# Kernel tuning notes

Hardware: AMD Instinct MI355X
Metric: run time of the kernel (lower is better)

The kernel has to match this reference:

```python
import jax, jax.numpy as jnp
import numpy as np

NUM_NODES = 100000
NUM_EDGES = 1600000
NUM_GRAPHS = 64
D_IN = 128
HID = 256
N_ATTR = 8
D_OUT = 1


def setup_inputs() -> dict:
    key = jax.random.key(0)
    ks = jax.random.split(key, 16)
    x = jax.random.normal(ks[0], (NUM_NODES, D_IN), dtype=jnp.float32)
    edge_index = jax.random.randint(ks[1], (2, NUM_EDGES), 0, NUM_NODES, dtype=jnp.int64)
    batch = jnp.sort(jax.random.randint(ks[2], (NUM_NODES,), 0, NUM_GRAPHS, dtype=jnp.int64))
    graph_attr = jax.random.normal(ks[3], (NUM_GRAPHS, N_ATTR), dtype=jnp.float32)
    def lin(k, fi, fo):
        s = 1.0 / np.sqrt(fi)
        return jax.random.uniform(k, (fi, fo), jnp.float32, -s, s)
    # SAGEConv: lin_l (applied to aggregated neighbors, has bias) + lin_r (root, no bias)
    W1l = lin(ks[4], D_IN, HID); b1 = jnp.zeros((HID,), jnp.float32)
    W1r = lin(ks[5], D_IN, HID)
    W2l = lin(ks[6], HID, HID); b2 = jnp.zeros((HID,), jnp.float32)
    W2r = lin(ks[7], HID, HID)
    Wf1 = lin(ks[8], HID + N_ATTR, HID); bf1 = jnp.zeros((HID,), jnp.float32)
    Wf2 = lin(ks[9], HID, D_OUT); bf2 = jnp.zeros((D_OUT,), jnp.float32)
    return {"x": x, "edge_index": edge_index, "batch": batch, "graph_attr": graph_attr,
            "W1l": W1l, "b1": b1, "W1r": W1r, "W2l": W2l, "b2": b2, "W2r": W2r,
            "Wf1": Wf1, "bf1": bf1, "Wf2": Wf2, "bf2": bf2}


def _mean_agg(h, src, dst, num_segments):
    # gather source features, scatter-mean into destination nodes
    s = jax.ops.segment_sum(h[src], dst, num_segments=num_segments)
    cnt = jax.ops.segment_sum(jnp.ones((src.shape[0], 1), h.dtype), dst, num_segments=num_segments)
    return s / jnp.maximum(cnt, 1.0)


def _sage(h, src, dst, Wl, b, Wr):
    agg = _mean_agg(h, src, dst, h.shape[0])
    return agg @ Wl + b + h @ Wr


def reference(x, edge_index, batch, graph_attr, W1l, b1, W1r, W2l, b2, W2r, Wf1, bf1, Wf2, bf2):
    src, dst = edge_index[0], edge_index[1]
    h = jax.nn.relu(_sage(x, src, dst, W1l, b1, W1r))
    h = _sage(h, src, dst, W2l, b2, W2r)
    # global mean pool over graphs
    gsum = jax.ops.segment_sum(h, batch, num_segments=NUM_GRAPHS)
    gcnt = jax.ops.segment_sum(jnp.ones((h.shape[0], 1), h.dtype), batch, num_segments=NUM_GRAPHS)
    g = gsum / jnp.maximum(gcnt, 1.0)
    g = jnp.concatenate([g, graph_attr.reshape(-1, N_ATTR)], axis=1)
    g = jax.nn.relu(g @ Wf1 + bf1)
    return g @ Wf2 + bf2
```

## Files before the change

### kernel.cpp

```cpp
#include <hip/hip_runtime.h>
#include <stdint.h>

#define NN 100000
#define NE 1600000
#define NG 64
#define DIN 128
#define HID 256
#define NATTR 8
#define NBK 391
#define CAP 6144
#define PCH 4096
#define BWW 25000
#define CB 12756
#define AEL 2048

typedef unsigned short u16;
typedef __attribute__((ext_vector_type(8))) short s16x8;
typedef __attribute__((ext_vector_type(4))) float f32x4;
typedef __attribute__((ext_vector_type(2))) float f32x2;
typedef __attribute__((ext_vector_type(4))) unsigned u32x4;

__device__ __forceinline__ int imaxi(int a, int b) { return a > b ? a : b; }
__device__ __forceinline__ u16 f2bf(float f) {
    unsigned u = __float_as_uint(f);
    return (u16)((u + 0x7fffu + ((u >> 16) & 1u)) >> 16);
}
__device__ __forceinline__ void gload16(const void* g, void* l) {
    __builtin_amdgcn_global_load_lds((const __attribute__((address_space(1))) void*)g,
                                     (__attribute__((address_space(3))) void*)l, 16, 0, 0);
}


__global__ void k_prep(const float4* __restrict__ x4, ushort4* __restrict__ xb4,
                       const float* __restrict__ W1l, const float* __restrict__ W1r,
                       u16* __restrict__ W1lt, u16* __restrict__ W1rt,
                       float4* __restrict__ P84, const int* __restrict__ batch,
                       int* __restrict__ goff, int* __restrict__ gcnt,
                       int* __restrict__ cursor) {
    int b = blockIdx.x, t = threadIdx.x;
    if (b < CB) {
        int i = b * 256 + t;
        const int NX4 = NN * DIN / 4;
        if (i < NX4) {
            float4 v = x4[i];
            ushort4 o;
            o.x = f2bf(v.x); o.y = f2bf(v.y); o.z = f2bf(v.z); o.w = f2bf(v.w);
            xb4[i] = o;
        } else {
            int j = i - NX4;
            if (j < 32768) {
                int n = j >> 7, k = j & 127;
                W1lt[j] = f2bf(W1l[k * HID + n]);
            } else if (j < 65536) {
                int jj = j - 32768;
                int n = jj >> 7, k = jj & 127;
                W1rt[jj] = f2bf(W1r[k * HID + n]);
            }
        }
    } else if (b < CB + 256) {
        int i = (b - CB) * 256 + t;
        P84[i] = make_float4(0.f, 0.f, 0.f, 0.f);
    } else {
        for (int i = t; i < NBK; i += 256) cursor[i] = 0;
        int g = t;
        if (g <= NG) {
            int lo = 0, hi = NN;
            while (lo < hi) {
                int mid = (lo + hi) >> 1;
                if (batch[mid] < g) lo = mid + 1; else hi = mid;
            }
            goff[g] = lo;
        }
        __syncthreads();
        if (g < NG) gcnt[g] = goff[g + 1] - goff[g];
    }
}


__global__ __launch_bounds__(256) void k_part(const int* __restrict__ ei,
                                              int* __restrict__ cursor,
                                              unsigned* __restrict__ pairs) {
    __shared__ unsigned spk[PCH];
    __shared__ unsigned short sbk[PCH];
    __shared__ int hist[NBK], gb[NBK];
    __shared__ int sc[512];
    int t = threadIdx.x;
    int c0 = blockIdx.x * PCH;
    int n = NE - c0; if (n > PCH) n = PCH;
    for (int i = t; i < NBK; i += 256) hist[i] = 0;
    __syncthreads();
    unsigned mypk[16]; unsigned short mybk[16]; int myoff[16];
#pragma unroll
    for (int j = 0; j < 16; j++) {
        int i = t + j * 256;
        myoff[j] = -1;
        if (i < n) {
            int e = c0 + i;
            unsigned d = (unsigned)__builtin_nontemporal_load(&ei[NE + e]);
            unsigned s = (unsigned)__builtin_nontemporal_load(&ei[e]);
            unsigned bk = d >> 8;
            mypk[j] = ((d & 255u) << 24) | s;
            mybk[j] = (unsigned short)bk;
            myoff[j] = atomicAdd(&hist[bk], 1);
        }
    }
    __syncthreads();
    sc[t] = (t < NBK) ? hist[t] : 0;
    sc[t + 256] = (t + 256 < NBK) ? hist[t + 256] : 0;
    __syncthreads();
    for (int off = 1; off < 512; off <<= 1) {
        int v0 = (t >= off) ? sc[t - off] : 0;
        int v1 = (t + 256 >= off) ? sc[t + 256 - off] : 0;
        __syncthreads();
        sc[t] += v0; sc[t + 256] += v1;
        __syncthreads();
    }
    if (t < NBK && hist[t] > 0) gb[t] = atomicAdd(&cursor[t], hist[t]);
    if (t + 256 < NBK && hist[t + 256] > 0)
        gb[t + 256] = atomicAdd(&cursor[t + 256], hist[t + 256]);
    __syncthreads();
#pragma unroll
    for (int j = 0; j < 16; j++) {
        if (myoff[j] >= 0) {
            int bk = mybk[j];
            int pos = sc[bk] - hist[bk] + myoff[j];
            spk[pos] = mypk[j];
            sbk[pos] = (unsigned short)bk;
        }
    }
    __syncthreads();
    for (int i = t; i < n; i += 256) {
        int bk = sbk[i];
        int local = gb[bk] + (i - (sc[bk] - hist[bk]));
        pairs[(size_t)bk * CAP + local] = spk[i];
    }
}


__global__ __launch_bounds__(256) void k_csr(const unsigned* __restrict__ pairs,
                                             const int* __restrict__ cursor,
                                             int* __restrict__ rowptr,
                                             unsigned* __restrict__ col) {
    __shared__ unsigned colL[CAP];
    __shared__ int csc[512];
    __shared__ int cnt[256], cur[256], sc[256];
    int b = blockIdx.x, t = threadIdx.x;
    csc[t] = (t < NBK) ? cursor[t] : 0;
    csc[t + 256] = (t + 256 < NBK) ? cursor[t + 256] : 0;
    __syncthreads();
    for (int off = 1; off < 512; off <<= 1) {
        int v0 = (t >= off) ? csc[t - off] : 0;
        int v1 = (t + 256 >= off) ? csc[t + 256 - off] : 0;
        __syncthreads();
        csc[t] += v0; csc[t + 256] += v1;
        __syncthreads();
    }
    int obase = (b == 0) ? 0 : csc[b - 1];
    int ecnt = cursor[b];
    const unsigned* pp = pairs + (size_t)b * CAP;
    cnt[t] = 0;
    __syncthreads();
    for (int i = t; i < ecnt; i += 256)
        atomicAdd(&cnt[pp[i] >> 24], 1);
    __syncthreads();
    sc[t] = cnt[t];
    __syncthreads();
    for (int off = 1; off < 256; off <<= 1) {
        int v = (t >= off) ? sc[t - off] : 0;
        __syncthreads();
        sc[t] += v;
        __syncthreads();
    }
    int lr = sc[t] - cnt[t];
    cur[t] = lr;
    int node = (b << 8) + t;
    if (node < NN) rowptr[node] = obase + lr;
    if (b == NBK - 1 && t == 0) rowptr[NN] = obase + ecnt;
    __syncthreads();
    for (int i = t; i < ecnt; i += 256) {
        unsigned p = pp[i];
        int dl = p >> 24;
        int pos = atomicAdd(&cur[dl], 1);
        int dd = cnt[dl]; if (dd > 32767) dd = 32767;
        colL[pos] = ((unsigned)dd << 17) | (p & 0xFFFFFFu);
    }
    __syncthreads();
    for (int i = t; i < ecnt; i += 256)
        col[obase + i] = colL[i];
}


__global__ __launch_bounds__(256) void k_agg(const uint4* __restrict__ xb4,
                                             uint4* __restrict__ agg4,
                                             const int* __restrict__ rowptr,
                                             const unsigned* __restrict__ col) {
    __shared__ unsigned scol[AEL];
    int t = threadIdx.x;
    int base = blockIdx.x * 4;
    int node = base + (t >> 6);
    int lane = t & 63;
    int qtr = lane >> 4, li = lane & 15;
    int s = rowptr[node], e = rowptr[node + 1];
    int bs = rowptr[base], be = rowptr[base + 4];
    int bn = be - bs;
    bool inl = bn <= AEL;
    if (inl)
        for (int j = t; j < bn; j += 256) scol[j] = col[bs + j];
    __syncthreads();

    f32x2 b01 = {0.f, 0.f}, b23 = {0.f, 0.f}, b45 = {0.f, 0.f}, b67 = {0.f, 0.f};

#define ACC8(V) do { \
        f32x2 p; \
        p[0] = __uint_as_float((V).x << 16); p[1] = __uint_as_float((V).x & 0xffff0000u); b01 += p; \
        p[0] = __uint_as_float((V).y << 16); p[1] = __uint_as_float((V).y & 0xffff0000u); b23 += p; \
        p[0] = __uint_as_float((V).z << 16); p[1] = __uint_as_float((V).z & 0xffff0000u); b45 += p; \
        p[0] = __uint_as_float((V).w << 16); p[1] = __uint_as_float((V).w & 0xffff0000u); b67 += p; \
    } while (0)

#define CL(X) scol[(X) - bs]
#define CG(X) col[X]
#define AGG_BODY(CIDX) do { \
        for (; i + 16 <= e; i += 16) { \
            unsigned c0 = (CIDX(i + qtr)) & 0x1FFFFu; \
            unsigned c1 = (CIDX(i + 4 + qtr)) & 0x1FFFFu; \
            unsigned c2 = (CIDX(i + 8 + qtr)) & 0x1FFFFu; \
            unsigned c3 = (CIDX(i + 12 + qtr)) & 0x1FFFFu; \
            uint4 w0 = xb4[(size_t)c0 * 16 + li]; \
            uint4 w1 = xb4[(size_t)c1 * 16 + li]; \
            uint4 w2 = xb4[(size_t)c2 * 16 + li]; \
            uint4 w3 = xb4[(size_t)c3 * 16 + li]; \
            ACC8(w0); ACC8(w1); ACC8(w2); ACC8(w3); \
        } \
        if (i + 8 <= e) { \
            unsigned c0 = (CIDX(i + qtr)) & 0x1FFFFu; \
            unsigned c1 = (CIDX(i + 4 + qtr)) & 0x1FFFFu; \
            uint4 w0 = xb4[(size_t)c0 * 16 + li]; \
            uint4 w1 = xb4[(size_t)c1 * 16 + li]; \
            ACC8(w0); ACC8(w1); \
            i += 8; \
        } \
        if (i + 4 <= e) { \
            unsigned c = (CIDX(i + qtr)) & 0x1FFFFu; \
            uint4 wv = xb4[(size_t)c * 16 + li]; \
            ACC8(wv); \
            i += 4; \
        } \
        if (i + qtr < e) { \
            unsigned c = (CIDX(i + qtr)) & 0x1FFFFu; \
            uint4 wv = xb4[(size_t)c * 16 + li]; \
            ACC8(wv); \
        } \
    } while (0)

    int i = s;
    if (inl) { AGG_BODY(CL); } else { AGG_BODY(CG); }
#undef AGG_BODY
#undef CL
#undef CG
#undef ACC8

    float a0 = b01[0], a1 = b01[1], a2 = b23[0], a3 = b23[1];
    float a4 = b45[0], a5 = b45[1], a6 = b67[0], a7 = b67[1];
    a0 += __shfl_xor(a0, 16); a1 += __shfl_xor(a1, 16);
    a2 += __shfl_xor(a2, 16); a3 += __shfl_xor(a3, 16);
    a4 += __shfl_xor(a4, 16); a5 += __shfl_xor(a5, 16);
    a6 += __shfl_xor(a6, 16); a7 += __shfl_xor(a7, 16);
    a0 += __shfl_xor(a0, 32); a1 += __shfl_xor(a1, 32);
    a2 += __shfl_xor(a2, 32); a3 += __shfl_xor(a3, 32);
    a4 += __shfl_xor(a4, 32); a5 += __shfl_xor(a5, 32);
    a6 += __shfl_xor(a6, 32); a7 += __shfl_xor(a7, 32);
    if (qtr == 0) {
        float inv = 1.f / (float)imaxi(e - s, 1);
        u32x4 ov;
        ov[0] = (((unsigned)f2bf(a1 * inv)) << 16) | (unsigned)f2bf(a0 * inv);
        ov[1] = (((unsigned)f2bf(a3 * inv)) << 16) | (unsigned)f2bf(a2 * inv);
        ov[2] = (((unsigned)f2bf(a5 * inv)) << 16) | (unsigned)f2bf(a4 * inv);
        ov[3] = (((unsigned)f2bf(a7 * inv)) << 16) | (unsigned)f2bf(a6 * inv);
        __builtin_nontemporal_store(ov, (u32x4*)&agg4[(size_t)node * 16 + li]);
    }
}


__global__ __launch_bounds__(512) void k_gemm1(
    const u16* __restrict__ agg1, const u16* __restrict__ xb,
    const u16* __restrict__ W1lt, const u16* __restrict__ W1rt,
    const float* __restrict__ b1, u16* __restrict__ h1t) {
    __shared__ u16 As[128][32];
    __shared__ u16 Bs[256][32];
    int t = threadIdx.x;
    int m0 = blockIdx.x * 128;
    int wave = t >> 6, lane = t & 63;
    int wm = wave & 1, wn = wave >> 1;
    int lm = lane & 15, quad = lane >> 4;
    int ar = t >> 2, aq = t & 3;
    f32x4 acc[4][4] = {};
    const u16* Ap = agg1;
    const u16* Bp = W1lt;
#pragma unroll
    for (int ph = 0; ph < 2; ph++) {
        for (int k0 = 0; k0 < DIN; k0 += 32) {
            gload16(Ap + (size_t)(m0 + ar) * DIN + k0 + aq * 8, &As[wave * 16][0]);
#pragma unroll
            for (int i = 0; i < 2; i++) {
                int r = (t + i * 512) >> 2;
                gload16(Bp + (size_t)r * DIN + k0 + aq * 8, &Bs[wave * 16 + i * 128][0]);
            }
            __syncthreads();
            s16x8 af[4], bfr[4];
#pragma unroll
            for (int i = 0; i < 4; i++) {
                af[i]  = *(const s16x8*)&As[wm * 64 + i * 16 + lm][quad * 8];
                bfr[i] = *(const s16x8*)&Bs[wn * 64 + i * 16 + lm][quad * 8];
            }
#pragma unroll
            for (int mi = 0; mi < 4; mi++)
#pragma unroll
                for (int ni = 0; ni < 4; ni++)
                    acc[mi][ni] = __builtin_amdgcn_mfma_f32_16x16x32_bf16(
                        af[mi], bfr[ni], acc[mi][ni], 0, 0, 0);
            __syncthreads();
        }
        Ap = xb; Bp = W1rt;
    }
#pragma unroll
    for (int ni = 0; ni < 4; ni++) {
        int colf = wn * 64 + ni * 16 + lm;
        float bias = b1[colf];
#pragma unroll
        for (int mi = 0; mi < 4; mi++) {
            int row = m0 + wm * 64 + mi * 16 + quad * 4;
            if (row < NN) {
                ushort4 o;
                o.x = f2bf(fmaxf(acc[mi][ni][0] + bias, 0.f));
                o.y = f2bf(fmaxf(acc[mi][ni][1] + bias, 0.f));
                o.z = f2bf(fmaxf(acc[mi][ni][2] + bias, 0.f));
                o.w = f2bf(fmaxf(acc[mi][ni][3] + bias, 0.f));
                *(ushort4*)(h1t + (size_t)colf * NN + row) = o;
            }
        }
    }
}


__global__ __launch_bounds__(256) void k_bw(
    const int* __restrict__ rowptr, const unsigned* __restrict__ col,
    const int* __restrict__ goff, u16* __restrict__ Wbt) {
    int b = blockIdx.x, t = threadIdx.x;
    if (b < 256) {
        __shared__ float bins[BWW];
        int g = b >> 2, w = b & 3;
        int lo = w * BWW;
        for (int i = t; i < BWW; i += 256) bins[i] = 0.f;
        __syncthreads();
        int ebeg = rowptr[goff[g]], eend = rowptr[goff[g + 1]];
        for (int i = ebeg + t; i < eend; i += 256) {
            unsigned c = col[i];
            unsigned sl = (c & 0x1FFFFu) - lo;
            if (sl < (unsigned)BWW) atomicAdd(&bins[sl], 1.0f / (float)(c >> 17));
        }
        __syncthreads();
        u16* out = Wbt + (size_t)g * NN + lo;
        for (int k = t; k < BWW / 4; k += 256) {
            ushort4 o;
            o.x = f2bf(bins[4 * k + 0]); o.y = f2bf(bins[4 * k + 1]);
            o.z = f2bf(bins[4 * k + 2]); o.w = f2bf(bins[4 * k + 3]);
            *(ushort4*)(out + 4 * k) = o;
        }
    } else {
        int g = b - 256;
        int a = goff[g], bnd = goff[g + 1];
        u16* out = Wbt + (size_t)(NG + g) * NN;
        for (int k = t; k < NN / 4; k += 256) {
            int c0 = 4 * k;
            ushort4 o;
            o.x = (c0 + 0 >= a && c0 + 0 < bnd) ? 0x3F80 : 0;
            o.y = (c0 + 1 >= a && c0 + 1 < bnd) ? 0x3F80 : 0;
            o.z = (c0 + 2 >= a && c0 + 2 < bnd) ? 0x3F80 : 0;
            o.w = (c0 + 3 >= a && c0 + 3 < bnd) ? 0x3F80 : 0;
            *(ushort4*)(out + c0) = o;
        }
    }
}


#define KCHUNK 512

__global__ __launch_bounds__(512) void k_poolg(
    const u16* __restrict__ Wbt, const u16* __restrict__ h1t, float* __restrict__ P8) {
    __shared__ u16 As[128][32];
    __shared__ u16 Bs[256][32];
    int t = threadIdx.x;
    int kbase = blockIdx.x * KCHUNK;
    int krem = NN - kbase;
    int ksteps = (krem < KCHUNK ? krem : KCHUNK) >> 5;
    int wave = t >> 6, lane = t & 63;
    int wm = wave & 1, wn = wave >> 1;
    int lm = lane & 15, quad = lane >> 4;
    int ar = t >> 2, aq = t & 3;
    float* P = P8 + (size_t)(blockIdx.x & 7) * 128 * HID;
    f32x4 acc[4][4] = {};
    for (int ks = 0; ks < ksteps; ks++) {
        int k0 = kbase + ks * 32;
        gload16(Wbt + (size_t)ar * NN + k0 + aq * 8, &As[wave * 16][0]);
#pragma unroll
        for (int i = 0; i < 2; i++) {
            int r = (t + i * 512) >> 2;
            gload16(h1t + (size_t)r * NN + k0 + aq * 8, &Bs[wave * 16 + i * 128][0]);
        }
        __syncthreads();
        s16x8 af[4], bfr[4];
#pragma unroll
        for (int i = 0; i < 4; i++) {
            af[i]  = *(const s16x8*)&As[wm * 64 + i * 16 + lm][quad * 8];
            bfr[i] = *(const s16x8*)&Bs[wn * 64 + i * 16 + lm][quad * 8];
        }
#pragma unroll
        for (int mi = 0; mi < 4; mi++)
#pragma unroll
            for (int ni = 0; ni < 4; ni++)
                acc[mi][ni] = __builtin_amdgcn_mfma_f32_16x16x32_bf16(
                    af[mi], bfr[ni], acc[mi][ni], 0, 0, 0);
        __syncthreads();
    }
#pragma unroll
    for (int mi = 0; mi < 4; mi++)
#pragma unroll
        for (int ni = 0; ni < 4; ni++) {
            int gcol = wm * 64 + mi * 16 + quad * 4;
            int feat = wn * 64 + ni * 16 + lm;
#pragma unroll
            for (int r = 0; r < 4; r++)
                atomicAdd(&P[(gcol + r) * HID + feat], acc[mi][ni][r]);
        }
}


__global__ void k_head(const float* __restrict__ P8, const int* __restrict__ gcnt,
                       const float* __restrict__ gattr,
                       const float* __restrict__ W2l, const float* __restrict__ b2,
                       const float* __restrict__ W2r,
                       const float* __restrict__ Wf1, const float* __restrict__ bf1,
                       const float* __restrict__ Wf2, const float* __restrict__ bf2v,
                       float* __restrict__ out) {
    __shared__ float pa[HID], ph[HID], gv[HID + NATTR];
    __shared__ float red[256];
    int g = blockIdx.x, t = threadIdx.x;
    float sa = 0.f, sh = 0.f;
#pragma unroll
    for (int c = 0; c < 8; c++) {
        sa += P8[(size_t)c * 128 * HID + g * HID + t];
        sh += P8[(size_t)c * 128 * HID + (NG + g) * HID + t];
    }
    pa[t] = sa; ph[t] = sh;
    __syncthreads();
    float s = 0.f;
    for (int k = 0; k < HID; k++)
        s += pa[k] * W2l[k * HID + t] + ph[k] * W2r[k * HID + t];
    float invc = 1.f / (float)imaxi(gcnt[g], 1);
    gv[t] = s * invc + b2[t];
    if (t < NATTR) gv[HID + t] = gattr[g * NATTR + t];
    __syncthreads();
    float h = bf1[t];
    for (int k = 0; k < HID + NATTR; k++) h += gv[k] * Wf1[k * HID + t];
    h = fmaxf(h, 0.f);
    red[t] = h * Wf2[t];
    __syncthreads();
    for (int off = 128; off > 0; off >>= 1) {
        if (t < off) red[t] += red[t + off];
        __syncthreads();
    }
    if (t == 0) out[g] = red[0] + bf2v[0];
}


extern "C" void kernel_launch(void* const* d_in, const int* in_sizes, int n_in,
                              void* d_out, int out_size, void* d_ws, size_t ws_size,
                              hipStream_t stream) {
    (void)in_sizes; (void)n_in; (void)out_size; (void)ws_size;
    const float* x     = (const float*)d_in[0];
    const int*   ei    = (const int*)d_in[1];
    const int*   batch = (const int*)d_in[2];
    const float* gattr = (const float*)d_in[3];
    const float* W1l   = (const float*)d_in[4];
    const float* b1    = (const float*)d_in[5];
    const float* W1r   = (const float*)d_in[6];
    const float* W2l   = (const float*)d_in[7];
    const float* b2    = (const float*)d_in[8];
    const float* W2r   = (const float*)d_in[9];
    const float* Wf1   = (const float*)d_in[10];
    const float* bf1   = (const float*)d_in[11];
    const float* Wf2   = (const float*)d_in[12];
    const float* bf2v  = (const float*)d_in[13];
    float* out = (float*)d_out;

    uint8_t* w = (uint8_t*)d_ws;
    size_t off = 0;
    auto alloc = [&](size_t bytes) -> void* {
        void* p = w + off;
        off += (bytes + 255) & ~(size_t)255;
        return p;
    };
    u16*      xb     = (u16*)alloc((size_t)NN * DIN * 2);
    u16*      agg1   = (u16*)alloc((size_t)NN * DIN * 2);
    u16*      h1t    = (u16*)alloc((size_t)NN * HID * 2);
    u16*      Wbt    = (u16*)alloc((size_t)128 * NN * 2);
    u16*      W1lt   = (u16*)alloc((size_t)HID * DIN * 2);
    u16*      W1rt   = (u16*)alloc((size_t)HID * DIN * 2);
    unsigned* pairs  = (unsigned*)alloc((size_t)NBK * CAP * 4);
    int*      rowptr = (int*)alloc((size_t)(NN + 1) * 4);
    unsigned* col    = (unsigned*)alloc((size_t)NE * 4);
    int*      cursor = (int*)alloc((NBK + 1) * 4);
    int*      goff   = (int*)alloc((NG + 1) * 4);
    int*      gcnt   = (int*)alloc(NG * 4);
    float*    P8     = (float*)alloc((size_t)8 * 128 * HID * 4);

    k_prep<<<CB + 257, 256, 0, stream>>>((const float4*)x, (ushort4*)xb, W1l, W1r,
                                         W1lt, W1rt, (float4*)P8, batch, goff, gcnt,
                                         cursor);

    k_part<<<(NE + PCH - 1) / PCH, 256, 0, stream>>>(ei, cursor, pairs);
    k_csr<<<NBK, 256, 0, stream>>>(pairs, cursor, rowptr, col);

    k_agg<<<NN / 4, 256, 0, stream>>>((const uint4*)xb, (uint4*)agg1, rowptr, col);
    k_gemm1<<<(NN + 127) / 128, 512, 0, stream>>>(agg1, xb, W1lt, W1rt, b1, h1t);

    k_bw<<<320, 256, 0, stream>>>(rowptr, col, goff, Wbt);
    k_poolg<<<(NN + KCHUNK - 1) / KCHUNK, 512, 0, stream>>>(Wbt, h1t, P8);

    k_head<<<NG, 256, 0, stream>>>(P8, gcnt, gattr, W2l, b2, W2r, Wf1, bf1, Wf2, bf2v, out);
}
```

Before: 370.8 us.

## Assign one node per quarter-wave in aggregation to drop cross-lane reductions

The aggregation kernel now maps each 16-lane quarter-wave to its own destination node (16 nodes per block) instead of spreading one node's edges across all four quarters of a wave. This removes the shuffle-based reduction at the end, makes every lane store its own output, and unrolls the neighbour loop to 8 outstanding gathers per lane. It also adds an occupancy hint to launch bounds and switches to a plain store. In exchange, quarters of a wave now loop over different degree counts, so lanes can diverge, and a single high-degree node keeps its quarter busy alone.

```diff
diff --git a/kernel.cpp b/kernel.cpp
--- a/kernel.cpp
+++ b/kernel.cpp
@@ -18,7 +18,6 @@
 typedef __attribute__((ext_vector_type(8))) short s16x8;
 typedef __attribute__((ext_vector_type(4))) float f32x4;
 typedef __attribute__((ext_vector_type(2))) float f32x2;
-typedef __attribute__((ext_vector_type(4))) unsigned u32x4;
 
 __device__ __forceinline__ int imaxi(int a, int b) { return a > b ? a : b; }
 __device__ __forceinline__ u16 f2bf(float f) {
@@ -190,18 +189,18 @@
 }
 
 
-__global__ __launch_bounds__(256) void k_agg(const uint4* __restrict__ xb4,
-                                             uint4* __restrict__ agg4,
-                                             const int* __restrict__ rowptr,
-                                             const unsigned* __restrict__ col) {
+__global__ __launch_bounds__(256, 8) void k_agg(const uint4* __restrict__ xb4,
+                                                uint4* __restrict__ agg4,
+                                                const int* __restrict__ rowptr,
+                                                const unsigned* __restrict__ col) {
     __shared__ unsigned scol[AEL];
     int t = threadIdx.x;
-    int base = blockIdx.x * 4;
-    int node = base + (t >> 6);
-    int lane = t & 63;
+    int base = blockIdx.x * 16;
+    int wave = t >> 6, lane = t & 63;
     int qtr = lane >> 4, li = lane & 15;
+    int node = base + (wave << 2) + qtr;
     int s = rowptr[node], e = rowptr[node + 1];
-    int bs = rowptr[base], be = rowptr[base + 4];
+    int bs = rowptr[base], be = rowptr[base + 16];
     int bn = be - bs;
     bool inl = bn <= AEL;
     if (inl)
@@ -209,6 +208,7 @@
     __syncthreads();
 
     f32x2 b01 = {0.f, 0.f}, b23 = {0.f, 0.f}, b45 = {0.f, 0.f}, b67 = {0.f, 0.f};
+    const uint4* xp = xb4 + li;
 
 #define ACC8(V) do { \
         f32x2 p; \
@@ -221,35 +221,37 @@
 #define CL(X) scol[(X) - bs]
 #define CG(X) col[X]
 #define AGG_BODY(CIDX) do { \
-        for (; i + 16 <= e; i += 16) { \
-            unsigned c0 = (CIDX(i + qtr)) & 0x1FFFFu; \
-            unsigned c1 = (CIDX(i + 4 + qtr)) & 0x1FFFFu; \
-            unsigned c2 = (CIDX(i + 8 + qtr)) & 0x1FFFFu; \
-            unsigned c3 = (CIDX(i + 12 + qtr)) & 0x1FFFFu; \
-            uint4 w0 = xb4[(size_t)c0 * 16 + li]; \
-            uint4 w1 = xb4[(size_t)c1 * 16 + li]; \
-            uint4 w2 = xb4[(size_t)c2 * 16 + li]; \
-            uint4 w3 = xb4[(size_t)c3 * 16 + li]; \
+        for (; i + 8 <= e; i += 8) { \
+            unsigned c0 = (CIDX(i + 0)) & 0x1FFFFu; \
+            unsigned c1 = (CIDX(i + 1)) & 0x1FFFFu; \
+            unsigned c2 = (CIDX(i + 2)) & 0x1FFFFu; \
+            unsigned c3 = (CIDX(i + 3)) & 0x1FFFFu; \
+            unsigned c4 = (CIDX(i + 4)) & 0x1FFFFu; \
+            unsigned c5 = (CIDX(i + 5)) & 0x1FFFFu; \
+            unsigned c6 = (CIDX(i + 6)) & 0x1FFFFu; \
+            unsigned c7 = (CIDX(i + 7)) & 0x1FFFFu; \
+            uint4 w0 = xp[(size_t)c0 * 16]; \
+            uint4 w1 = xp[(size_t)c1 * 16]; \
+            uint4 w2 = xp[(size_t)c2 * 16]; \
+            uint4 w3 = xp[(size_t)c3 * 16]; \
+            uint4 w4 = xp[(size_t)c4 * 16]; \
+            uint4 w5 = xp[(size_t)c5 * 16]; \
+            uint4 w6 = xp[(size_t)c6 * 16]; \
+            uint4 w7 = xp[(size_t)c7 * 16]; \
             ACC8(w0); ACC8(w1); ACC8(w2); ACC8(w3); \
+            ACC8(w4); ACC8(w5); ACC8(w6); ACC8(w7); \
         } \
-        if (i + 8 <= e) { \
-            unsigned c0 = (CIDX(i + qtr)) & 0x1FFFFu; \
-            unsigned c1 = (CIDX(i + 4 + qtr)) & 0x1FFFFu; \
-            uint4 w0 = xb4[(size_t)c0 * 16 + li]; \
-            uint4 w1 = xb4[(size_t)c1 * 16 + li]; \
+        for (; i + 2 <= e; i += 2) { \
+            unsigned c0 = (CIDX(i + 0)) & 0x1FFFFu; \
+            unsigned c1 = (CIDX(i + 1)) & 0x1FFFFu; \
+            uint4 w0 = xp[(size_t)c0 * 16]; \
+            uint4 w1 = xp[(size_t)c1 * 16]; \
             ACC8(w0); ACC8(w1); \
-            i += 8; \
         } \
-        if (i + 4 <= e) { \
-            unsigned c = (CIDX(i + qtr)) & 0x1FFFFu; \
-            uint4 wv = xb4[(size_t)c * 16 + li]; \
-            ACC8(wv); \
-            i += 4; \
-        } \
-        if (i + qtr < e) { \
-            unsigned c = (CIDX(i + qtr)) & 0x1FFFFu; \
-            uint4 wv = xb4[(size_t)c * 16 + li]; \
-            ACC8(wv); \
+        if (i < e) { \
+            unsigned c0 = (CIDX(i)) & 0x1FFFFu; \
+            uint4 w0 = xp[(size_t)c0 * 16]; \
+            ACC8(w0); \
         } \
     } while (0)
 
@@ -260,25 +262,13 @@
 #undef CG
 #undef ACC8
 
-    float a0 = b01[0], a1 = b01[1], a2 = b23[0], a3 = b23[1];
-    float a4 = b45[0], a5 = b45[1], a6 = b67[0], a7 = b67[1];
-    a0 += __shfl_xor(a0, 16); a1 += __shfl_xor(a1, 16);
-    a2 += __shfl_xor(a2, 16); a3 += __shfl_xor(a3, 16);
-    a4 += __shfl_xor(a4, 16); a5 += __shfl_xor(a5, 16);
-    a6 += __shfl_xor(a6, 16); a7 += __shfl_xor(a7, 16);
-    a0 += __shfl_xor(a0, 32); a1 += __shfl_xor(a1, 32);
-    a2 += __shfl_xor(a2, 32); a3 += __shfl_xor(a3, 32);
-    a4 += __shfl_xor(a4, 32); a5 += __shfl_xor(a5, 32);
-    a6 += __shfl_xor(a6, 32); a7 += __shfl_xor(a7, 32);
-    if (qtr == 0) {
-        float inv = 1.f / (float)imaxi(e - s, 1);
-        u32x4 ov;
-        ov[0] = (((unsigned)f2bf(a1 * inv)) << 16) | (unsigned)f2bf(a0 * inv);
-        ov[1] = (((unsigned)f2bf(a3 * inv)) << 16) | (unsigned)f2bf(a2 * inv);
-        ov[2] = (((unsigned)f2bf(a5 * inv)) << 16) | (unsigned)f2bf(a4 * inv);
-        ov[3] = (((unsigned)f2bf(a7 * inv)) << 16) | (unsigned)f2bf(a6 * inv);
-        __builtin_nontemporal_store(ov, (u32x4*)&agg4[(size_t)node * 16 + li]);
-    }
+    float inv = 1.f / (float)imaxi(e - s, 1);
+    uint4 o;
+    o.x = (((unsigned)f2bf(b01[1] * inv)) << 16) | (unsigned)f2bf(b01[0] * inv);
+    o.y = (((unsigned)f2bf(b23[1] * inv)) << 16) | (unsigned)f2bf(b23[0] * inv);
+    o.z = (((unsigned)f2bf(b45[1] * inv)) << 16) | (unsigned)f2bf(b45[0] * inv);
+    o.w = (((unsigned)f2bf(b67[1] * inv)) << 16) | (unsigned)f2bf(b67[0] * inv);
+    agg4[(size_t)node * 16 + li] = o;
 }
 
 
@@ -522,7 +512,7 @@
     k_part<<<(NE + PCH - 1) / PCH, 256, 0, stream>>>(ei, cursor, pairs);
     k_csr<<<NBK, 256, 0, stream>>>(pairs, cursor, rowptr, col);
 
-    k_agg<<<NN / 4, 256, 0, stream>>>((const uint4*)xb, (uint4*)agg1, rowptr, col);
+    k_agg<<<NN / 16, 256, 0, stream>>>((const uint4*)xb, (uint4*)agg1, rowptr, col);
     k_gemm1<<<(NN + 127) / 128, 512, 0, stream>>>(agg1, xb, W1lt, W1rt, b1, h1t);
 
     k_bw<<<320, 256, 0, stream>>>(rowptr, col, goff, Wbt);
```

Result: no change. 364.2 us (-1.8%).
